# Kernel optimization log

Hardware: AMD Instinct MI355X
Metric: run time of the kernel (lower is better)

## Reference

```python
import jax, jax.numpy as jnp
import numpy as np
import math

B, T, S, D, H = 2, 1024, 1024, 1024, 16
DH = D // H


def setup_inputs() -> dict:
    key = jax.random.key(0)
    ks = jax.random.split(key, 13)
    scale = 1.0 / math.sqrt(D)
    inp = {
        "q": jax.random.normal(ks[0], (B, T, D), jnp.float32),
        "k": jax.random.normal(ks[1], (B, S, D), jnp.float32),
        "v": jax.random.normal(ks[2], (B, S, D), jnp.float32),
        # causal mask: True means masked
        "attn_mask": jnp.broadcast_to(
            jnp.triu(jnp.ones((T, S), jnp.bool_), k=1)[None, None], (B, 1, T, S)
        ),
        "attn_bias": jax.random.normal(ks[3], (B, H, T, S), jnp.float32),
        "Wq": jax.random.normal(ks[4], (D, D), jnp.float32) * scale,
        "bq": jnp.zeros((D,), jnp.float32),
        "Wk": jax.random.normal(ks[5], (D, D), jnp.float32) * scale,
        "bk": jnp.zeros((D,), jnp.float32),
        "Wv": jax.random.normal(ks[6], (D, D), jnp.float32) * scale,
        "bv": jnp.zeros((D,), jnp.float32),
        "Wo": jax.random.normal(ks[7], (D, D), jnp.float32) * scale,
        "bo": jnp.zeros((D,), jnp.float32),
        "bias_scale": jnp.asarray(0.5, jnp.float32),
    }
    return inp


def reference(q, k, v, attn_mask, attn_bias, Wq, bq, Wk, bk, Wv, bv, Wo, bo, bias_scale):
    # projections (torch Linear convention: x @ W.T + b), split heads
    qh = (q @ Wq.T + bq).reshape(B, T, H, DH)   # (B,T,H,DH)
    kh = (k @ Wk.T + bk).reshape(B, S, H, DH)
    vh = (v @ Wv.T + bv).reshape(B, S, H, DH)

    scores = jnp.einsum("bthd,bshd->bhts", qh, kh) / math.sqrt(DH)  # (B,H,T,S)
    scores = jnp.clip(scores, -80.0, 80.0)
    scores = jnp.where(attn_mask, -jnp.inf, scores)  # mask broadcasts over H
    attn = jax.nn.softmax(scores, axis=-1)

    # post-softmax multiplicative bias + renormalize
    scale = 1.0 + bias_scale * jnp.tanh(attn_bias)
    attn = attn * jnp.maximum(scale, 1e-9)
    attn = attn / (jnp.sum(attn, axis=-1, keepdims=True) + 1e-9)

    # dropout p=0.0 (eval) -> identity
    out = jnp.einsum("bhts,bshd->bthd", attn, vh).reshape(B, T, D)
    out = out @ Wo.T + bo
    return out, attn
```

## Files before the change

kernel.cpp:

```cpp
#include <hip/hip_runtime.h>
#include <hip/hip_bf16.h>
#include <math.h>

#define BB 2
#define TT 1024
#define SS 1024
#define DD 1024
#define HH 16
#define DH 64

typedef __attribute__((ext_vector_type(8))) short bf16x8;
typedef __attribute__((ext_vector_type(4))) float f32x4;
typedef unsigned short ushort_t;

#define AS3(p) ((__attribute__((address_space(3))) unsigned int*)(p))
#define AS1(p) ((const __attribute__((address_space(1))) unsigned int*)(p))

__device__ __forceinline__ unsigned short f2b(float f) {
    union { float f; unsigned u; } x; x.f = f;
    unsigned r = x.u + 0x7FFFu + ((x.u >> 16) & 1u);
    return (unsigned short)(r >> 16);
}

__global__ __launch_bounds__(256) void cvt3_kernel(
    const float* __restrict__ a, const float* __restrict__ b, const float* __restrict__ c,
    ushort_t* __restrict__ oa, ushort_t* __restrict__ ob, ushort_t* __restrict__ oc)
{
    const float* src = (blockIdx.y == 0) ? a : (blockIdx.y == 1) ? b : c;
    ushort_t* dst    = (blockIdx.y == 0) ? oa : (blockIdx.y == 1) ? ob : oc;
    size_t i = ((size_t)blockIdx.x * 256 + threadIdx.x) * 8;
    float4 v0 = *(const float4*)&src[i];
    float4 v1 = *(const float4*)&src[i + 4];
    uint4 o;
    o.x = f2b(v0.x) | ((unsigned)f2b(v0.y) << 16);
    o.y = f2b(v0.z) | ((unsigned)f2b(v0.w) << 16);
    o.z = f2b(v1.x) | ((unsigned)f2b(v1.y) << 16);
    o.w = f2b(v1.z) | ((unsigned)f2b(v1.w) << 16);
    *(uint4*)&dst[i] = o;
}

__global__ __launch_bounds__(256) void cvt4_kernel(
    const float* __restrict__ a, const float* __restrict__ b,
    const float* __restrict__ c, const float* __restrict__ d,
    ushort_t* __restrict__ oa, ushort_t* __restrict__ ob,
    ushort_t* __restrict__ oc, ushort_t* __restrict__ od)
{
    const float* src = (blockIdx.y == 0) ? a : (blockIdx.y == 1) ? b : (blockIdx.y == 2) ? c : d;
    ushort_t* dst    = (blockIdx.y == 0) ? oa : (blockIdx.y == 1) ? ob : (blockIdx.y == 2) ? oc : od;
    size_t i = ((size_t)blockIdx.x * 256 + threadIdx.x) * 8;
    float4 v0 = *(const float4*)&src[i];
    float4 v1 = *(const float4*)&src[i + 4];
    uint4 o;
    o.x = f2b(v0.x) | ((unsigned)f2b(v0.y) << 16);
    o.y = f2b(v0.z) | ((unsigned)f2b(v0.w) << 16);
    o.z = f2b(v1.x) | ((unsigned)f2b(v1.y) << 16);
    o.w = f2b(v1.z) | ((unsigned)f2b(v1.w) << 16);
    *(uint4*)&dst[i] = o;
}

__device__ __forceinline__ void gemm128_mainloop(
    const ushort_t* __restrict__ A,
    const ushort_t* __restrict__ Bw,
    int K, ushort_t* Asm, ushort_t* Bsm, f32x4 acc[4][4])
{
    const int tid = threadIdx.x;
    const int wave = tid >> 6, lane = tid & 63;
    const int sr = lane >> 2;
    const int gc = (lane & 3) ^ ((lane >> 3) & 3);
    const int l15 = lane & 15, q = lane >> 4;
    const int mblk = (wave >> 1) * 64, nblk = (wave & 1) * 64;

    for (int k0 = 0; k0 < K; k0 += 32) {
        #pragma unroll
        for (int o = 0; o < 2; o++) {
            int r0 = (wave * 2 + o) * 16;
            __builtin_amdgcn_global_load_lds(AS1(A + (size_t)(r0 + sr) * K + k0 + gc * 8),
                                             AS3(Asm + r0 * 32), 16, 0, 0);
            __builtin_amdgcn_global_load_lds(AS1(Bw + (size_t)(r0 + sr) * K + k0 + gc * 8),
                                             AS3(Bsm + r0 * 32), 16, 0, 0);
        }
        __syncthreads();

        bf16x8 av[4], bv[4];
        #pragma unroll
        for (int mi = 0; mi < 4; mi++) {
            int r = mblk + mi * 16 + l15;
            av[mi] = *(const bf16x8*)&Asm[r * 32 + (q ^ ((r >> 1) & 3)) * 8];
        }
        #pragma unroll
        for (int ni = 0; ni < 4; ni++) {
            int r = nblk + ni * 16 + l15;
            bv[ni] = *(const bf16x8*)&Bsm[r * 32 + (q ^ ((r >> 1) & 3)) * 8];
        }
        #pragma unroll
        for (int mi = 0; mi < 4; mi++)
            #pragma unroll
            for (int ni = 0; ni < 4; ni++)
                acc[mi][ni] = __builtin_amdgcn_mfma_f32_16x16x32_bf16(av[mi], bv[ni], acc[mi][ni], 0, 0, 0);
        __syncthreads();
    }
}

__global__ __launch_bounds__(256) void proj_gemm(
    const ushort_t* __restrict__ qb, const ushort_t* __restrict__ kb, const ushort_t* __restrict__ vb,
    const ushort_t* __restrict__ Wqb, const ushort_t* __restrict__ Wkb, const ushort_t* __restrict__ Wvb,
    const float* __restrict__ bq, const float* __restrict__ bk, const float* __restrict__ bv,
    ushort_t* __restrict__ qh, ushort_t* __restrict__ kh, ushort_t* __restrict__ vh)
{
    __shared__ ushort_t Asm[128 * 32];
    __shared__ ushort_t Bsm[128 * 32];
    const int z = blockIdx.z;
    const ushort_t* A = (z == 0) ? qb : (z == 1) ? kb : vb;
    const ushort_t* W = (z == 0) ? Wqb : (z == 1) ? Wkb : Wvb;
    const float* bias = (z == 0) ? bq : (z == 1) ? bk : bv;
    ushort_t* Y = (z == 0) ? qh : (z == 1) ? kh : vh;

    const int bm = blockIdx.y * 128, bn = blockIdx.x * 128;
    f32x4 acc[4][4];
    #pragma unroll
    for (int i = 0; i < 4; i++)
        #pragma unroll
        for (int j = 0; j < 4; j++) acc[i][j] = (f32x4)(0.f);

    gemm128_mainloop(A + (size_t)bm * DD, W + (size_t)bn * DD, DD, Asm, Bsm, acc);

    const int lane = threadIdx.x & 63, wave = threadIdx.x >> 6;
    const int mblk = (wave >> 1) * 64, nblk = (wave & 1) * 64;
    const int l15 = lane & 15, q = lane >> 4;
    #pragma unroll
    for (int mi = 0; mi < 4; mi++) {
        #pragma unroll
        for (int ni = 0; ni < 4; ni++) {
            int col = bn + nblk + ni * 16 + l15;
            float bcol = bias[col];
            #pragma unroll
            for (int r = 0; r < 4; r++) {
                int row = bm + mblk + mi * 16 + q * 4 + r;
                Y[(size_t)row * DD + col] = f2b(acc[mi][ni][r] + bcol);
            }
        }
    }
}

__global__ __launch_bounds__(256) void oproj_gemm(
    const ushort_t* __restrict__ A, const ushort_t* __restrict__ W,
    const float* __restrict__ bias, float* __restrict__ Y)
{
    __shared__ ushort_t Asm[128 * 32];
    __shared__ ushort_t Bsm[128 * 32];
    const int bm = blockIdx.y * 128, bn = blockIdx.x * 128;
    f32x4 acc[4][4];
    #pragma unroll
    for (int i = 0; i < 4; i++)
        #pragma unroll
        for (int j = 0; j < 4; j++) acc[i][j] = (f32x4)(0.f);

    gemm128_mainloop(A + (size_t)bm * DD, W + (size_t)bn * DD, DD, Asm, Bsm, acc);

    const int lane = threadIdx.x & 63, wave = threadIdx.x >> 6;
    const int mblk = (wave >> 1) * 64, nblk = (wave & 1) * 64;
    const int l15 = lane & 15, q = lane >> 4;
    #pragma unroll
    for (int mi = 0; mi < 4; mi++) {
        #pragma unroll
        for (int ni = 0; ni < 4; ni++) {
            int col = bn + nblk + ni * 16 + l15;
            float bcol = bias[col];
            #pragma unroll
            for (int r = 0; r < 4; r++) {
                int row = bm + mblk + mi * 16 + q * 4 + r;
                Y[(size_t)row * DD + col] = acc[mi][ni][r] + bcol;
            }
        }
    }
}

__global__ __launch_bounds__(256) void transpose_v(
    const ushort_t* __restrict__ vh, ushort_t* __restrict__ vT)
{
    __shared__ ushort_t Ls[64][72];
    const int s0 = blockIdx.x * 64;
    const int bh = blockIdx.y;
    const int b = bh >> 4, h = bh & 15;
    const int tid = threadIdx.x;
    const int r = tid >> 2, c16 = (tid & 3) * 16;

    const ushort_t* src = &vh[((size_t)(b * SS + s0 + r) * HH + h) * DH + c16];
    uint4 u0 = *(const uint4*)src;
    uint4 u1 = *(const uint4*)(src + 8);
    ushort_t tmp[16];
    *(uint4*)&tmp[0] = u0; *(uint4*)&tmp[8] = u1;
    #pragma unroll
    for (int j = 0; j < 16; j++) Ls[c16 + j][r] = tmp[j];
    __syncthreads();

    const int dh = r;
    uint4 w0 = *(const uint4*)&Ls[dh][c16];
    uint4 w1 = *(const uint4*)&Ls[dh][c16 + 8];
    ushort_t* dst = &vT[((size_t)bh * DH + dh) * SS + s0 + c16];
    *(uint4*)dst = w0;
    *(uint4*)(dst + 8) = w1;
}

__global__ __launch_bounds__(256) void scores_mfma(
    const ushort_t* __restrict__ qh, const ushort_t* __restrict__ kh,
    float* __restrict__ attn)
{
    __shared__ ushort_t Qs[128 * 64];
    __shared__ ushort_t Ks[128 * 64];

    int idx = blockIdx.x, ti = 0;
    while (idx >= ti + 1) { idx -= ti + 1; ti++; }
    const int si = idx;
    const int bh = blockIdx.y;
    const int b = bh >> 4, h = bh & 15;
    const int t0 = ti * 128, s0 = si * 128;

    const int tid = threadIdx.x;
    const int wave = tid >> 6, lane = tid & 63;
    const int sr8 = lane >> 3;
    const int gc8 = (lane & 7) ^ sr8;

    #pragma unroll
    for (int o = 0; o < 4; o++) {
        int r0 = (wave * 4 + o) * 8;
        int r = r0 + sr8;
        __builtin_amdgcn_global_load_lds(
            AS1(qh + ((size_t)(b * TT + t0 + r) * HH + h) * DH + gc8 * 8),
            AS3(Qs + r0 * 64), 16, 0, 0);
        __builtin_amdgcn_global_load_lds(
            AS1(kh + ((size_t)(b * SS + s0 + r) * HH + h) * DH + gc8 * 8),
            AS3(Ks + r0 * 64), 16, 0, 0);
    }
    __syncthreads();

    const int l15 = lane & 15, q = lane >> 4;
    const int tblk = (wave >> 1) * 64, sblk = (wave & 1) * 64;
    f32x4 acc[4][4];
    #pragma unroll
    for (int i = 0; i < 4; i++)
        #pragma unroll
        for (int j = 0; j < 4; j++) acc[i][j] = (f32x4)(0.f);

    #pragma unroll
    for (int ks = 0; ks < 2; ks++) {
        bf16x8 av[4], bv[4];
        #pragma unroll
        for (int mi = 0; mi < 4; mi++) {
            int r = tblk + mi * 16 + l15;
            av[mi] = *(const bf16x8*)&Qs[r * 64 + ((ks * 4 + q) ^ (r & 7)) * 8];
        }
        #pragma unroll
        for (int ni = 0; ni < 4; ni++) {
            int r = sblk + ni * 16 + l15;
            bv[ni] = *(const bf16x8*)&Ks[r * 64 + ((ks * 4 + q) ^ (r & 7)) * 8];
        }
        #pragma unroll
        for (int mi = 0; mi < 4; mi++)
            #pragma unroll
            for (int ni = 0; ni < 4; ni++)
                acc[mi][ni] = __builtin_amdgcn_mfma_f32_16x16x32_bf16(av[mi], bv[ni], acc[mi][ni], 0, 0, 0);
    }

    #pragma unroll
    for (int mi = 0; mi < 4; mi++) {
        #pragma unroll
        for (int ni = 0; ni < 4; ni++) {
            int scol = s0 + sblk + ni * 16 + l15;
            #pragma unroll
            for (int r = 0; r < 4; r++) {
                int t = t0 + tblk + mi * 16 + q * 4 + r;
                float v = acc[mi][ni][r] * 0.125f;
                v = fminf(fmaxf(v, -80.f), 80.f);
                attn[((size_t)bh * TT + t) * SS + scol] = v;
            }
        }
    }
}

__global__ __launch_bounds__(256) void softmax_bias_wave(
    const float* __restrict__ attn_bias, const float* __restrict__ bias_scale_p,
    float* __restrict__ attn)
{
    const int wave = threadIdx.x >> 6, lane = threadIdx.x & 63;
    const int row = blockIdx.x * 4 + wave;
    const int t = row & (TT - 1);

    float* prow = attn + (size_t)row * SS;
    const float* brow = attn_bias + (size_t)row * SS;
    const float bscale = bias_scale_p[0];

    const int nc = (t >> 8) + 1;

    float v[16];
    float m = -INFINITY;
    #pragma unroll
    for (int c = 0; c < 4; c++) {
        const int s0 = c * 256 + lane * 4;
        if (c < nc) {
            float4 rv = *(const float4*)&prow[s0];
            v[c * 4 + 0] = (s0     <= t) ? rv.x : -INFINITY;
            v[c * 4 + 1] = (s0 + 1 <= t) ? rv.y : -INFINITY;
            v[c * 4 + 2] = (s0 + 2 <= t) ? rv.z : -INFINITY;
            v[c * 4 + 3] = (s0 + 3 <= t) ? rv.w : -INFINITY;
            m = fmaxf(m, fmaxf(fmaxf(v[c*4], v[c*4+1]), fmaxf(v[c*4+2], v[c*4+3])));
        } else {
            v[c * 4 + 0] = -INFINITY; v[c * 4 + 1] = -INFINITY;
            v[c * 4 + 2] = -INFINITY; v[c * 4 + 3] = -INFINITY;
        }
    }
    #pragma unroll
    for (int off = 1; off < 64; off <<= 1)
        m = fmaxf(m, __shfl_xor(m, off));

    float w[16];
    float P = 0.f, Wn = 0.f;
    #pragma unroll
    for (int c = 0; c < 4; c++) {
        const int s0 = c * 256 + lane * 4;
        if (c < nc) {
            float4 bv = *(const float4*)&brow[s0];
            float bx[4] = {bv.x, bv.y, bv.z, bv.w};
            #pragma unroll
            for (int j = 0; j < 4; j++) {
                float vv = v[c * 4 + j];
                float p = (vv > -INFINITY) ? __expf(vv - m) : 0.f;
                float e = __expf(-2.f * fabsf(bx[j]));
                float th = copysignf((1.f - e) / (1.f + e), bx[j]);
                float sc = fmaxf(1.f + bscale * th, 1e-9f);
                float ww = p * sc;
                w[c * 4 + j] = ww;
                P += p; Wn += ww;
            }
        } else {
            w[c * 4 + 0] = 0.f; w[c * 4 + 1] = 0.f;
            w[c * 4 + 2] = 0.f; w[c * 4 + 3] = 0.f;
        }
    }
    #pragma unroll
    for (int off = 1; off < 64; off <<= 1) {
        P  += __shfl_xor(P, off);
        Wn += __shfl_xor(Wn, off);
    }
    const float inv = 1.f / (Wn + 1e-9f * P);

    #pragma unroll
    for (int c = 0; c < 4; c++) {
        const int s0 = c * 256 + lane * 4;
        float4 o;
        o.x = w[c * 4 + 0] * inv; o.y = w[c * 4 + 1] * inv;
        o.z = w[c * 4 + 2] * inv; o.w = w[c * 4 + 3] * inv;
        *(float4*)&prow[s0] = o;
    }
}

__global__ __launch_bounds__(256) void av_mfma(
    const float* __restrict__ attn, const ushort_t* __restrict__ vT,
    ushort_t* __restrict__ ao)
{
    __shared__ ushort_t Asm[64 * 32];
    __shared__ ushort_t Vsm[64 * 32];

    const int tb = blockIdx.x;
    const int bh = blockIdx.y;
    const int b = bh >> 4, h = bh & 15;
    const int t0 = tb * 64;
    const int nsteps = (tb + 1) * 2;

    const int tid = threadIdx.x;
    const int wave = tid >> 6, lane = tid & 63;
    const int ar = tid >> 2, aq = tid & 3;
    const int aslot = aq ^ ((ar >> 1) & 3);
    const int vsr = lane >> 2;
    const int vgc = (lane & 3) ^ ((lane >> 3) & 3);
    const int l15 = lane & 15, q = lane >> 4;

    f32x4 acc[4];
    #pragma unroll
    for (int i = 0; i < 4; i++) acc[i] = (f32x4)(0.f);

    for (int st = 0; st < nsteps; st++) {
        const int s0 = st * 32;
        {
            const float* src = &attn[((size_t)bh * TT + t0 + ar) * SS + s0 + aq * 8];
            float4 u0 = *(const float4*)src;
            float4 u1 = *(const float4*)(src + 4);
            uint4 o;
            o.x = f2b(u0.x) | ((unsigned)f2b(u0.y) << 16);
            o.y = f2b(u0.z) | ((unsigned)f2b(u0.w) << 16);
            o.z = f2b(u1.x) | ((unsigned)f2b(u1.y) << 16);
            o.w = f2b(u1.z) | ((unsigned)f2b(u1.w) << 16);
            *(uint4*)&Asm[ar * 32 + aslot * 8] = o;
        }
        {
            int r0 = wave * 16;
            __builtin_amdgcn_global_load_lds(
                AS1(vT + ((size_t)bh * DH + r0 + vsr) * SS + s0 + vgc * 8),
                AS3(Vsm + r0 * 32), 16, 0, 0);
        }
        __syncthreads();

        bf16x8 a0, bv[4];
        {
            int r = wave * 16 + l15;
            a0 = *(const bf16x8*)&Asm[r * 32 + (q ^ ((r >> 1) & 3)) * 8];
        }
        #pragma unroll
        for (int ni = 0; ni < 4; ni++) {
            int r = ni * 16 + l15;
            bv[ni] = *(const bf16x8*)&Vsm[r * 32 + (q ^ ((r >> 1) & 3)) * 8];
        }
        #pragma unroll
        for (int ni = 0; ni < 4; ni++)
            acc[ni] = __builtin_amdgcn_mfma_f32_16x16x32_bf16(a0, bv[ni], acc[ni], 0, 0, 0);
        __syncthreads();
    }

    #pragma unroll
    for (int ni = 0; ni < 4; ni++) {
        int dh = ni * 16 + l15;
        #pragma unroll
        for (int r = 0; r < 4; r++) {
            int t = t0 + wave * 16 + q * 4 + r;
            ao[(size_t)(b * TT + t) * DD + h * DH + dh] = f2b(acc[ni][r]);
        }
    }
}

extern "C" void kernel_launch(void* const* d_in, const int* in_sizes, int n_in,
                              void* d_out, int out_size, void* d_ws, size_t ws_size,
                              hipStream_t stream)
{
    const float* q   = (const float*)d_in[0];
    const float* k   = (const float*)d_in[1];
    const float* v   = (const float*)d_in[2];
    const float* attn_bias = (const float*)d_in[4];
    const float* Wq = (const float*)d_in[5];
    const float* bq = (const float*)d_in[6];
    const float* Wk = (const float*)d_in[7];
    const float* bk = (const float*)d_in[8];
    const float* Wv = (const float*)d_in[9];
    const float* bv = (const float*)d_in[10];
    const float* Wo = (const float*)d_in[11];
    const float* bo = (const float*)d_in[12];
    const float* bscale = (const float*)d_in[13];

    char* base = (char*)d_ws;
    ushort_t* qb  = (ushort_t*)(base + (0ull << 20));
    ushort_t* kb  = (ushort_t*)(base + (4ull << 20));
    ushort_t* vb  = (ushort_t*)(base + (8ull << 20));
    ushort_t* Wqb = (ushort_t*)(base + (12ull << 20));
    ushort_t* Wkb = (ushort_t*)(base + (14ull << 20));
    ushort_t* Wvb = (ushort_t*)(base + (16ull << 20));
    ushort_t* Wob = (ushort_t*)(base + (18ull << 20));
    ushort_t* qhb = (ushort_t*)(base + (20ull << 20));
    ushort_t* khb = (ushort_t*)(base + (24ull << 20));
    ushort_t* vhb = (ushort_t*)(base + (28ull << 20));
    ushort_t* vT  = qb;
    ushort_t* aob = kb;

    float* out  = (float*)d_out;
    float* attn = out + (size_t)BB * TT * DD;

    cvt3_kernel<<<dim3(1024, 3), 256, 0, stream>>>(q, k, v, qb, kb, vb);
    cvt4_kernel<<<dim3(512, 4), 256, 0, stream>>>(Wq, Wk, Wv, Wo, Wqb, Wkb, Wvb, Wob);
    proj_gemm<<<dim3(8, 16, 3), 256, 0, stream>>>(qb, kb, vb, Wqb, Wkb, Wvb,
                                                  bq, bk, bv, qhb, khb, vhb);
    transpose_v<<<dim3(16, 32), 256, 0, stream>>>(vhb, vT);
    scores_mfma<<<dim3(36, 32), 256, 0, stream>>>(qhb, khb, attn);
    softmax_bias_wave<<<dim3(8192), 256, 0, stream>>>(attn_bias, bscale, attn);
    av_mfma<<<dim3(16, 32), 256, 0, stream>>>(attn, vT, aob);
    oproj_gemm<<<dim3(8, 16), 256, 0, stream>>>(aob, Wob, bo, out);
}
```

Measured before the change: 374.9 us.

## Double K tile in GEMMs and software-pipeline AV kernel with double-buffered V

The shared GEMM mainloop now loads 64-wide K tiles with an 8-way XOR swizzle, so there are half as many barriers per K. The attention-times-V kernel drops the LDS staging of attention probabilities: each lane loads its own fp32 rows into registers and converts them with packed v_cvt_pk_bf16_f32. V tiles are double-buffered in LDS so the next step's loads overlap the current MFMAs. Causal blocks are also issued in reverse order so the longest ones start first. LDS use per block goes up, which may reduce occupancy.

```diff
diff --git a/kernel.cpp b/kernel.cpp
--- a/kernel.cpp
+++ b/kernel.cpp
@@ -20,6 +20,15 @@
     union { float f; unsigned u; } x; x.f = f;
     unsigned r = x.u + 0x7FFFu + ((x.u >> 16) & 1u);
     return (unsigned short)(r >> 16);
+}
+
+__device__ __forceinline__ bf16x8 pack_bf16x8(float4 a, float4 b) {
+    union { unsigned u[4]; bf16x8 v; } r;
+    asm("v_cvt_pk_bf16_f32 %0, %1, %2" : "=v"(r.u[0]) : "v"(a.x), "v"(a.y));
+    asm("v_cvt_pk_bf16_f32 %0, %1, %2" : "=v"(r.u[1]) : "v"(a.z), "v"(a.w));
+    asm("v_cvt_pk_bf16_f32 %0, %1, %2" : "=v"(r.u[2]) : "v"(b.x), "v"(b.y));
+    asm("v_cvt_pk_bf16_f32 %0, %1, %2" : "=v"(r.u[3]) : "v"(b.z), "v"(b.w));
+    return r.v;
 }
 
 __global__ __launch_bounds__(256) void cvt3_kernel(
@@ -65,38 +74,41 @@
 {
     const int tid = threadIdx.x;
     const int wave = tid >> 6, lane = tid & 63;
-    const int sr = lane >> 2;
-    const int gc = (lane & 3) ^ ((lane >> 3) & 3);
+    const int sr8 = lane >> 3;
+    const int gc8 = (lane & 7) ^ sr8;
     const int l15 = lane & 15, q = lane >> 4;
     const int mblk = (wave >> 1) * 64, nblk = (wave & 1) * 64;
 
-    for (int k0 = 0; k0 < K; k0 += 32) {
-        #pragma unroll
-        for (int o = 0; o < 2; o++) {
-            int r0 = (wave * 2 + o) * 16;
-            __builtin_amdgcn_global_load_lds(AS1(A + (size_t)(r0 + sr) * K + k0 + gc * 8),
-                                             AS3(Asm + r0 * 32), 16, 0, 0);
-            __builtin_amdgcn_global_load_lds(AS1(Bw + (size_t)(r0 + sr) * K + k0 + gc * 8),
-                                             AS3(Bsm + r0 * 32), 16, 0, 0);
+    for (int k0 = 0; k0 < K; k0 += 64) {
+        #pragma unroll
+        for (int o = 0; o < 4; o++) {
+            int r0 = wave * 32 + o * 8;
+            __builtin_amdgcn_global_load_lds(AS1(A + (size_t)(r0 + sr8) * K + k0 + gc8 * 8),
+                                             AS3(Asm + r0 * 64), 16, 0, 0);
+            __builtin_amdgcn_global_load_lds(AS1(Bw + (size_t)(r0 + sr8) * K + k0 + gc8 * 8),
+                                             AS3(Bsm + r0 * 64), 16, 0, 0);
         }
         __syncthreads();
 
-        bf16x8 av[4], bv[4];
-        #pragma unroll
-        for (int mi = 0; mi < 4; mi++) {
-            int r = mblk + mi * 16 + l15;
-            av[mi] = *(const bf16x8*)&Asm[r * 32 + (q ^ ((r >> 1) & 3)) * 8];
-        }
-        #pragma unroll
-        for (int ni = 0; ni < 4; ni++) {
-            int r = nblk + ni * 16 + l15;
-            bv[ni] = *(const bf16x8*)&Bsm[r * 32 + (q ^ ((r >> 1) & 3)) * 8];
-        }
-        #pragma unroll
-        for (int mi = 0; mi < 4; mi++)
-            #pragma unroll
-            for (int ni = 0; ni < 4; ni++)
-                acc[mi][ni] = __builtin_amdgcn_mfma_f32_16x16x32_bf16(av[mi], bv[ni], acc[mi][ni], 0, 0, 0);
+        #pragma unroll
+        for (int ks = 0; ks < 2; ks++) {
+            bf16x8 av[4], bv[4];
+            #pragma unroll
+            for (int mi = 0; mi < 4; mi++) {
+                int r = mblk + mi * 16 + l15;
+                av[mi] = *(const bf16x8*)&Asm[r * 64 + ((ks * 4 + q) ^ (r & 7)) * 8];
+            }
+            #pragma unroll
+            for (int ni = 0; ni < 4; ni++) {
+                int r = nblk + ni * 16 + l15;
+                bv[ni] = *(const bf16x8*)&Bsm[r * 64 + ((ks * 4 + q) ^ (r & 7)) * 8];
+            }
+            #pragma unroll
+            for (int mi = 0; mi < 4; mi++)
+                #pragma unroll
+                for (int ni = 0; ni < 4; ni++)
+                    acc[mi][ni] = __builtin_amdgcn_mfma_f32_16x16x32_bf16(av[mi], bv[ni], acc[mi][ni], 0, 0, 0);
+        }
         __syncthreads();
     }
 }
@@ -107,8 +119,8 @@
     const float* __restrict__ bq, const float* __restrict__ bk, const float* __restrict__ bv,
     ushort_t* __restrict__ qh, ushort_t* __restrict__ kh, ushort_t* __restrict__ vh)
 {
-    __shared__ ushort_t Asm[128 * 32];
-    __shared__ ushort_t Bsm[128 * 32];
+    __shared__ ushort_t Asm[128 * 64];
+    __shared__ ushort_t Bsm[128 * 64];
     const int z = blockIdx.z;
     const ushort_t* A = (z == 0) ? qb : (z == 1) ? kb : vb;
     const ushort_t* W = (z == 0) ? Wqb : (z == 1) ? Wkb : Wvb;
@@ -146,8 +158,8 @@
     const ushort_t* __restrict__ A, const ushort_t* __restrict__ W,
     const float* __restrict__ bias, float* __restrict__ Y)
 {
-    __shared__ ushort_t Asm[128 * 32];
-    __shared__ ushort_t Bsm[128 * 32];
+    __shared__ ushort_t Asm[128 * 64];
+    __shared__ ushort_t Bsm[128 * 64];
     const int bm = blockIdx.y * 128, bn = blockIdx.x * 128;
     f32x4 acc[4][4];
     #pragma unroll
@@ -358,63 +370,75 @@
     const float* __restrict__ attn, const ushort_t* __restrict__ vT,
     ushort_t* __restrict__ ao)
 {
-    __shared__ ushort_t Asm[64 * 32];
-    __shared__ ushort_t Vsm[64 * 32];
-
-    const int tb = blockIdx.x;
+    __shared__ ushort_t Vsm[2][64 * 64];
+
+    const int tb = (int)gridDim.x - 1 - (int)blockIdx.x;
     const int bh = blockIdx.y;
     const int b = bh >> 4, h = bh & 15;
     const int t0 = tb * 64;
-    const int nsteps = (tb + 1) * 2;
+    const int nsteps = tb + 1;
 
     const int tid = threadIdx.x;
     const int wave = tid >> 6, lane = tid & 63;
-    const int ar = tid >> 2, aq = tid & 3;
-    const int aslot = aq ^ ((ar >> 1) & 3);
-    const int vsr = lane >> 2;
-    const int vgc = (lane & 3) ^ ((lane >> 3) & 3);
+    const int sr8 = lane >> 3, gc8 = (lane & 7) ^ sr8;
     const int l15 = lane & 15, q = lane >> 4;
 
+    const float* arow = attn + ((size_t)bh * TT + t0 + wave * 16 + l15) * SS + q * 8;
+    const ushort_t* vbase = vT + (size_t)bh * DH * SS;
+
     f32x4 acc[4];
     #pragma unroll
     for (int i = 0; i < 4; i++) acc[i] = (f32x4)(0.f);
 
-    for (int st = 0; st < nsteps; st++) {
-        const int s0 = st * 32;
-        {
-            const float* src = &attn[((size_t)bh * TT + t0 + ar) * SS + s0 + aq * 8];
-            float4 u0 = *(const float4*)src;
-            float4 u1 = *(const float4*)(src + 4);
-            uint4 o;
-            o.x = f2b(u0.x) | ((unsigned)f2b(u0.y) << 16);
-            o.y = f2b(u0.z) | ((unsigned)f2b(u0.w) << 16);
-            o.z = f2b(u1.x) | ((unsigned)f2b(u1.y) << 16);
-            o.w = f2b(u1.z) | ((unsigned)f2b(u1.w) << 16);
-            *(uint4*)&Asm[ar * 32 + aslot * 8] = o;
-        }
-        {
-            int r0 = wave * 16;
-            __builtin_amdgcn_global_load_lds(
-                AS1(vT + ((size_t)bh * DH + r0 + vsr) * SS + s0 + vgc * 8),
-                AS3(Vsm + r0 * 32), 16, 0, 0);
-        }
+#define STAGE_V(sidx, buf) do {                                               \
+        int s0_ = (sidx) * 64;                                                \
+        _Pragma("unroll")                                                     \
+        for (int o = 0; o < 2; o++) {                                         \
+            int r0 = wave * 16 + o * 8;                                       \
+            __builtin_amdgcn_global_load_lds(                                 \
+                AS1(vbase + (size_t)(r0 + sr8) * SS + s0_ + gc8 * 8),         \
+                AS3(&Vsm[buf][r0 * 64]), 16, 0, 0);                           \
+        } } while (0)
+
+#define LOAD_A(sidx, dst) do {                                                \
+        const float* p_ = arow + (sidx) * 64;                                 \
+        dst[0] = *(const float4*)(p_);                                        \
+        dst[1] = *(const float4*)(p_ + 4);                                    \
+        dst[2] = *(const float4*)(p_ + 32);                                   \
+        dst[3] = *(const float4*)(p_ + 36); } while (0)
+
+#define COMPUTE(buf, ax) do {                                                 \
+        bf16x8 af0 = pack_bf16x8(ax[0], ax[1]);                               \
+        bf16x8 af1 = pack_bf16x8(ax[2], ax[3]);                               \
+        _Pragma("unroll")                                                     \
+        for (int ni = 0; ni < 4; ni++) {                                      \
+            int rv = ni * 16 + l15;                                           \
+            bf16x8 b0 = *(const bf16x8*)&Vsm[buf][rv * 64 + ((q) ^ (rv & 7)) * 8];       \
+            bf16x8 b1 = *(const bf16x8*)&Vsm[buf][rv * 64 + ((4 + q) ^ (rv & 7)) * 8];   \
+            acc[ni] = __builtin_amdgcn_mfma_f32_16x16x32_bf16(af0, b0, acc[ni], 0, 0, 0);\
+            acc[ni] = __builtin_amdgcn_mfma_f32_16x16x32_bf16(af1, b1, acc[ni], 0, 0, 0);\
+        } } while (0)
+
+    float4 aA[4], aB[4];
+    STAGE_V(0, 0);
+    LOAD_A(0, aA);
+    __syncthreads();
+
+    int st = 0;
+    while (true) {
+        if (st + 1 < nsteps) { STAGE_V(st + 1, 1); LOAD_A(st + 1, aB); }
+        COMPUTE(0, aA);
         __syncthreads();
-
-        bf16x8 a0, bv[4];
-        {
-            int r = wave * 16 + l15;
-            a0 = *(const bf16x8*)&Asm[r * 32 + (q ^ ((r >> 1) & 3)) * 8];
-        }
-        #pragma unroll
-        for (int ni = 0; ni < 4; ni++) {
-            int r = ni * 16 + l15;
-            bv[ni] = *(const bf16x8*)&Vsm[r * 32 + (q ^ ((r >> 1) & 3)) * 8];
-        }
-        #pragma unroll
-        for (int ni = 0; ni < 4; ni++)
-            acc[ni] = __builtin_amdgcn_mfma_f32_16x16x32_bf16(a0, bv[ni], acc[ni], 0, 0, 0);
+        if (++st == nsteps) break;
+        if (st + 1 < nsteps) { STAGE_V(st + 1, 0); LOAD_A(st + 1, aA); }
+        COMPUTE(1, aB);
         __syncthreads();
-    }
+        if (++st == nsteps) break;
+    }
+
+#undef STAGE_V
+#undef LOAD_A
+#undef COMPUTE
 
     #pragma unroll
     for (int ni = 0; ni < 4; ni++) {
```

New measurement: 374.8 us. Within noise of the previous version (-0.0%).
